# Optimization experiments

Hardware: AMD Instinct MI355X
Metric: run time of the kernel (lower is better)

## Reference

```python
import jax, jax.numpy as jnp
import numpy as np

IN_FEATURES = 4096
OUT_FEATURES = 8192
GROUP_SIZE = 16
NUM_GROUPS = IN_FEATURES * OUT_FEATURES // GROUP_SIZE  # 2_097_152


def block_dequantize_2bit(packed, normalization):
    # packed: [G, group_size//4] int32 holding uint8 values; norm: [G, 1] fp16
    shifts = jnp.arange(4, dtype=packed.dtype) * 2  # bit offsets 0,2,4,6
    # unpacked column 4k+i comes from packed column k, bits 2i..2i+1
    u = ((packed[:, :, None] >> shifts) & 3).astype(jnp.float32)  # [G, gs/4, 4]
    u = u.reshape(packed.shape[0], -1)  # [G, group_size]
    norm = normalization.astype(jnp.float32)
    return (u / 3.0) * (2.0 * norm) - norm  # [G, group_size]


def setup_inputs() -> dict:
    key = jax.random.key(0)
    k_x, k_q, k_n, k_b = jax.random.split(key, 4)
    x = jax.random.normal(k_x, (256, IN_FEATURES), dtype=jnp.float32)
    # packed 2-bit weights: random bytes (store as int32 for clean bit ops in jax)
    weight_q2 = jax.random.randint(k_q, (NUM_GROUPS, GROUP_SIZE // 4), 0, 256, dtype=jnp.int32)
    # per-group normalization (abs-max), positive, fp16 as in the module buffer
    weight_norm = (jax.random.uniform(k_n, (NUM_GROUPS, 1), dtype=jnp.float32) * 0.05 + 1e-4).astype(jnp.float16)
    bias = jax.random.normal(k_b, (OUT_FEATURES,), dtype=jnp.float32) * 0.01
    return {"x": x, "weight_q2": weight_q2, "weight_norm": weight_norm, "bias": bias}


def reference(x, weight_q2, weight_norm, bias):
    weight = block_dequantize_2bit(weight_q2, weight_norm).reshape(OUT_FEATURES, IN_FEATURES)
    return jnp.dot(x.astype(jnp.float32), weight.T) + bias
```

## Files before the change

kernel.cpp:

```cpp
#include <hip/hip_runtime.h>
#include <hip/hip_bf16.h>
#include <hip/hip_fp16.h>

#define IN_F   4096
#define OUT_F  8192
#define M_ROWS 256

typedef __attribute__((ext_vector_type(8))) short  short8;
typedef __attribute__((ext_vector_type(4))) float  float4v;

__device__ inline unsigned int pack_bf16(float lo, float hi) {
    return __builtin_amdgcn_perm(__float_as_uint(hi), __float_as_uint(lo), 0x07060302u);
}

__global__ void cvt_x_kernel(const float* __restrict__ x, unsigned short* __restrict__ xb) {
    int i = blockIdx.x * blockDim.x + threadIdx.x;
    if (i < (M_ROWS * IN_F) / 4) {
        float4 v = ((const float4*)x)[i];
        uint2 o;
        o.x = pack_bf16(v.x, v.y);
        o.y = pack_bf16(v.z, v.w);
        ((uint2*)xb)[i] = o;
    }
}

template <bool XB>
__global__ __launch_bounds__(256) void gemm2bit_kernel(
    const float*           __restrict__ xf,
    const unsigned short*  __restrict__ xb,
    const int*             __restrict__ wq,
    const void*            __restrict__ wnorm,
    const float*           __restrict__ bias,
    float*                 __restrict__ out)
{
    __shared__ unsigned short ldsA[64 * 40];
    __shared__ unsigned short ldsB[64 * 40];

    const int t    = threadIdx.x;
    const int n0   = blockIdx.x * 64;
    const int m0   = blockIdx.y * 64;
    const int wave = t >> 6;
    const int lane = t & 63;
    const int wrow = wave >> 1;
    const int wcol = wave & 1;
    const int l15  = lane & 15;
    const int quad = lane >> 4;

    const float cand0 = *(const float*)wnorm;
    const bool  nf32  = (cand0 > 1e-5f && cand0 < 0.1f);

    const int srow = t >> 2;
    const int sc8  = (t & 3) * 8;

    float4v acc[2][2] = {};

    for (int k0 = 0; k0 < IN_F; k0 += 32) {
        uint4 aval;
        if (XB) {
            aval = *(const uint4*)(xb + (m0 + srow) * IN_F + k0 + sc8);
        } else {
            const float* p = xf + (m0 + srow) * IN_F + k0 + sc8;
            float4 v0 = ((const float4*)p)[0];
            float4 v1 = ((const float4*)p)[1];
            aval.x = pack_bf16(v0.x, v0.y);
            aval.y = pack_bf16(v0.z, v0.w);
            aval.z = pack_bf16(v1.x, v1.y);
            aval.w = pack_bf16(v1.z, v1.w);
        }

        int2  q = *(const int2*)(wq + (n0 + srow) * (IN_F / 4) + ((k0 + sc8) >> 2));
        const int g = (n0 + srow) * (IN_F / 16) + ((k0 + sc8) >> 4);
        float norm;
        if (nf32) norm = ((const float*)wnorm)[g];
        else      norm = __half2float(((const __half*)wnorm)[g]);
        float s  = norm * (2.0f / 3.0f);
        float tn = -norm;
        float f[8];
#pragma unroll
        for (int i = 0; i < 4; ++i)
            f[i] = fmaf((float)((q.x >> (2 * i)) & 3), s, tn);
#pragma unroll
        for (int i = 0; i < 4; ++i)
            f[4 + i] = fmaf((float)((q.y >> (2 * i)) & 3), s, tn);
        uint4 bval;
        bval.x = pack_bf16(f[0], f[1]);
        bval.y = pack_bf16(f[2], f[3]);
        bval.z = pack_bf16(f[4], f[5]);
        bval.w = pack_bf16(f[6], f[7]);

        __syncthreads();
        *(uint4*)&ldsA[srow * 40 + sc8] = aval;
        *(uint4*)&ldsB[srow * 40 + sc8] = bval;
        __syncthreads();

        short8 a0 = *(const short8*)&ldsA[(wrow * 32 +  0 + l15) * 40 + quad * 8];
        short8 a1 = *(const short8*)&ldsA[(wrow * 32 + 16 + l15) * 40 + quad * 8];
        short8 b0 = *(const short8*)&ldsB[(wcol * 32 +  0 + l15) * 40 + quad * 8];
        short8 b1 = *(const short8*)&ldsB[(wcol * 32 + 16 + l15) * 40 + quad * 8];

        acc[0][0] = __builtin_amdgcn_mfma_f32_16x16x32_bf16(a0, b0, acc[0][0], 0, 0, 0);
        acc[0][1] = __builtin_amdgcn_mfma_f32_16x16x32_bf16(a0, b1, acc[0][1], 0, 0, 0);
        acc[1][0] = __builtin_amdgcn_mfma_f32_16x16x32_bf16(a1, b0, acc[1][0], 0, 0, 0);
        acc[1][1] = __builtin_amdgcn_mfma_f32_16x16x32_bf16(a1, b1, acc[1][1], 0, 0, 0);
    }

#pragma unroll
    for (int j = 0; j < 2; ++j) {
        const int col = n0 + wcol * 32 + j * 16 + l15;
        const float bv = bias[col];
#pragma unroll
        for (int i = 0; i < 2; ++i) {
            const int row0 = m0 + wrow * 32 + i * 16 + quad * 4;
#pragma unroll
            for (int r = 0; r < 4; ++r) {
                out[(row0 + r) * OUT_F + col] = acc[i][j][r] + bv;
            }
        }
    }
}

extern "C" void kernel_launch(void* const* d_in, const int* in_sizes, int n_in,
                              void* d_out, int out_size, void* d_ws, size_t ws_size,
                              hipStream_t stream) {
    const float*          x    = (const float*)d_in[0];
    const int*            wq   = (const int*)d_in[1];
    const void*           wn   = (const void*)d_in[2];
    const float*          bias = (const float*)d_in[3];
    float*                out  = (float*)d_out;

    const bool use_ws = ws_size >= (size_t)(M_ROWS * IN_F * sizeof(unsigned short));

    dim3 grid(OUT_F / 64, M_ROWS / 64);

    if (use_ws) {
        unsigned short* xb = (unsigned short*)d_ws;
        cvt_x_kernel<<<dim3((M_ROWS * IN_F / 4 + 255) / 256), 256, 0, stream>>>(x, xb);
        gemm2bit_kernel<true><<<grid, 256, 0, stream>>>(nullptr, xb, wq, wn, bias, out);
    } else {
        gemm2bit_kernel<false><<<grid, 256, 0, stream>>>(x, nullptr, wq, wn, bias, out);
    }
}
```

Measured before the change: 152.9 us.

## Double-buffer LDS with register prefetch, K=64 steps and XOR-swizzled layout

Raises the K step per iteration from 32 to 64, prefetches the next tile's activations, packed weights and norms into registers while the current tile is dequantized and multiplied, and alternates between two LDS buffers so each step needs one barrier instead of two. The LDS layout moves from padded rows to an XOR swizzle to avoid bank conflicts, and launch bounds request two blocks per CU. The goal is to hide global load latency and cut synchronization overhead, at the cost of more registers and LDS per block.

```diff
diff --git a/kernel.cpp b/kernel.cpp
--- a/kernel.cpp
+++ b/kernel.cpp
@@ -13,6 +13,10 @@
     return __builtin_amdgcn_perm(__float_as_uint(hi), __float_as_uint(lo), 0x07060302u);
 }
 
+__device__ inline int sw_idx(int row, int kchunk) {
+    return row * 64 + ((kchunk ^ (row & 7)) << 3);
+}
+
 __global__ void cvt_x_kernel(const float* __restrict__ x, unsigned short* __restrict__ xb) {
     int i = blockIdx.x * blockDim.x + threadIdx.x;
     if (i < (M_ROWS * IN_F) / 4) {
@@ -24,8 +28,17 @@
     }
 }
 
+__device__ inline void load_a16_f32(const float* __restrict__ p, uint4& o0, uint4& o1) {
+    float4 v0 = ((const float4*)p)[0], v1 = ((const float4*)p)[1];
+    float4 v2 = ((const float4*)p)[2], v3 = ((const float4*)p)[3];
+    o0.x = pack_bf16(v0.x, v0.y); o0.y = pack_bf16(v0.z, v0.w);
+    o0.z = pack_bf16(v1.x, v1.y); o0.w = pack_bf16(v1.z, v1.w);
+    o1.x = pack_bf16(v2.x, v2.y); o1.y = pack_bf16(v2.z, v2.w);
+    o1.z = pack_bf16(v3.x, v3.y); o1.w = pack_bf16(v3.z, v3.w);
+}
+
 template <bool XB>
-__global__ __launch_bounds__(256) void gemm2bit_kernel(
+__global__ __launch_bounds__(256, 2) void gemm2bit_kernel(
     const float*           __restrict__ xf,
     const unsigned short*  __restrict__ xb,
     const int*             __restrict__ wq,
@@ -33,84 +46,125 @@
     const float*           __restrict__ bias,
     float*                 __restrict__ out)
 {
-    __shared__ unsigned short ldsA[64 * 40];
-    __shared__ unsigned short ldsB[64 * 40];
+    __shared__ unsigned short lds[2][2][64 * 64];
 
     const int t    = threadIdx.x;
     const int n0   = blockIdx.x * 64;
     const int m0   = blockIdx.y * 64;
     const int wave = t >> 6;
     const int lane = t & 63;
-    const int wrow = wave >> 1;
-    const int wcol = wave & 1;
     const int l15  = lane & 15;
     const int quad = lane >> 4;
+    const int wm   = (wave >> 1) * 32;
+    const int wn   = (wave & 1) * 32;
 
     const float cand0 = *(const float*)wnorm;
     const bool  nf32  = (cand0 > 1e-5f && cand0 < 0.1f);
 
     const int srow = t >> 2;
-    const int sc8  = (t & 3) * 8;
+    const int skc  = t & 3;
+    const int c0   = skc * 2;
+    const int wO0  = sw_idx(srow, c0);
+    const int wO1  = sw_idx(srow, c0 + 1);
+
+    int fa0[2], fa1[2], fb0[2], fb1[2];
+#pragma unroll
+    for (int kk = 0; kk < 2; ++kk) {
+        fa0[kk] = sw_idx(wm +      l15, kk * 4 + quad);
+        fa1[kk] = sw_idx(wm + 16 + l15, kk * 4 + quad);
+        fb0[kk] = sw_idx(wn +      l15, kk * 4 + quad);
+        fb1[kk] = sw_idx(wn + 16 + l15, kk * 4 + quad);
+    }
+
+    const int arow = m0 + srow;
+    const int brow = n0 + srow;
+    const float*          nrmF = (const float*)wnorm;
+    const __half*         nrmH = (const __half*)wnorm;
 
     float4v acc[2][2] = {};
 
-    for (int k0 = 0; k0 < IN_F; k0 += 32) {
-        uint4 aval;
+    uint4 aN0, aN1; int4 qN; float nN;
+    {
         if (XB) {
-            aval = *(const uint4*)(xb + (m0 + srow) * IN_F + k0 + sc8);
+            const unsigned short* p = xb + arow * IN_F + skc * 16;
+            aN0 = *(const uint4*)p;
+            aN1 = *(const uint4*)(p + 8);
         } else {
-            const float* p = xf + (m0 + srow) * IN_F + k0 + sc8;
-            float4 v0 = ((const float4*)p)[0];
-            float4 v1 = ((const float4*)p)[1];
-            aval.x = pack_bf16(v0.x, v0.y);
-            aval.y = pack_bf16(v0.z, v0.w);
-            aval.z = pack_bf16(v1.x, v1.y);
-            aval.w = pack_bf16(v1.z, v1.w);
+            load_a16_f32(xf + arow * IN_F + skc * 16, aN0, aN1);
         }
+        qN = *(const int4*)(wq + brow * (IN_F / 4) + skc * 4);
+        const int gi = brow * (IN_F / 16) + skc;
+        nN = nf32 ? nrmF[gi] : __half2float(nrmH[gi]);
+    }
 
-        int2  q = *(const int2*)(wq + (n0 + srow) * (IN_F / 4) + ((k0 + sc8) >> 2));
-        const int g = (n0 + srow) * (IN_F / 16) + ((k0 + sc8) >> 4);
-        float norm;
-        if (nf32) norm = ((const float*)wnorm)[g];
-        else      norm = __half2float(((const __half*)wnorm)[g]);
-        float s  = norm * (2.0f / 3.0f);
-        float tn = -norm;
-        float f[8];
+    for (int ito = 0; ito < 32; ++ito) {
 #pragma unroll
-        for (int i = 0; i < 4; ++i)
-            f[i] = fmaf((float)((q.x >> (2 * i)) & 3), s, tn);
+        for (int half = 0; half < 2; ++half) {
+            const int it = ito * 2 + half;
+
+            uint4 aC0 = aN0, aC1 = aN1;
+            int4  qC  = qN;
+            float nC  = nN;
+
+            if (it < 63) {
+                const int kn = (it + 1) << 6;
+                if (XB) {
+                    const unsigned short* p = xb + arow * IN_F + kn + skc * 16;
+                    aN0 = *(const uint4*)p;
+                    aN1 = *(const uint4*)(p + 8);
+                } else {
+                    load_a16_f32(xf + arow * IN_F + kn + skc * 16, aN0, aN1);
+                }
+                qN = *(const int4*)(wq + brow * (IN_F / 4) + (kn >> 2) + skc * 4);
+                const int gi = brow * (IN_F / 16) + (kn >> 4) + skc;
+                nN = nf32 ? nrmF[gi] : __half2float(nrmH[gi]);
+            }
+
+            const float s = nC * (2.0f / 3.0f);
+            float f[16];
+            const int qa[4] = {qC.x, qC.y, qC.z, qC.w};
 #pragma unroll
-        for (int i = 0; i < 4; ++i)
-            f[4 + i] = fmaf((float)((q.y >> (2 * i)) & 3), s, tn);
-        uint4 bval;
-        bval.x = pack_bf16(f[0], f[1]);
-        bval.y = pack_bf16(f[2], f[3]);
-        bval.z = pack_bf16(f[4], f[5]);
-        bval.w = pack_bf16(f[6], f[7]);
+            for (int bq = 0; bq < 4; ++bq) {
+#pragma unroll
+                for (int i = 0; i < 4; ++i)
+                    f[bq * 4 + i] = fmaf((float)((qa[bq] >> (2 * i)) & 3), s, -nC);
+            }
+            uint4 bv0, bv1;
+            bv0.x = pack_bf16(f[0],  f[1]);   bv0.y = pack_bf16(f[2],  f[3]);
+            bv0.z = pack_bf16(f[4],  f[5]);   bv0.w = pack_bf16(f[6],  f[7]);
+            bv1.x = pack_bf16(f[8],  f[9]);   bv1.y = pack_bf16(f[10], f[11]);
+            bv1.z = pack_bf16(f[12], f[13]);  bv1.w = pack_bf16(f[14], f[15]);
 
-        __syncthreads();
-        *(uint4*)&ldsA[srow * 40 + sc8] = aval;
-        *(uint4*)&ldsB[srow * 40 + sc8] = bval;
-        __syncthreads();
+            unsigned short* LA = lds[half][0];
+            unsigned short* LB = lds[half][1];
+            *(uint4*)&LA[wO0] = aC0;
+            *(uint4*)&LA[wO1] = aC1;
+            *(uint4*)&LB[wO0] = bv0;
+            *(uint4*)&LB[wO1] = bv1;
 
-        short8 a0 = *(const short8*)&ldsA[(wrow * 32 +  0 + l15) * 40 + quad * 8];
-        short8 a1 = *(const short8*)&ldsA[(wrow * 32 + 16 + l15) * 40 + quad * 8];
-        short8 b0 = *(const short8*)&ldsB[(wcol * 32 +  0 + l15) * 40 + quad * 8];
-        short8 b1 = *(const short8*)&ldsB[(wcol * 32 + 16 + l15) * 40 + quad * 8];
+            __syncthreads();
 
-        acc[0][0] = __builtin_amdgcn_mfma_f32_16x16x32_bf16(a0, b0, acc[0][0], 0, 0, 0);
-        acc[0][1] = __builtin_amdgcn_mfma_f32_16x16x32_bf16(a0, b1, acc[0][1], 0, 0, 0);
-        acc[1][0] = __builtin_amdgcn_mfma_f32_16x16x32_bf16(a1, b0, acc[1][0], 0, 0, 0);
-        acc[1][1] = __builtin_amdgcn_mfma_f32_16x16x32_bf16(a1, b1, acc[1][1], 0, 0, 0);
+#pragma unroll
+            for (int kk = 0; kk < 2; ++kk) {
+                short8 a0 = *(const short8*)&LA[fa0[kk]];
+                short8 a1 = *(const short8*)&LA[fa1[kk]];
+                short8 b0 = *(const short8*)&LB[fb0[kk]];
+                short8 b1 = *(const short8*)&LB[fb1[kk]];
+                acc[0][0] = __builtin_amdgcn_mfma_f32_16x16x32_bf16(a0, b0, acc[0][0], 0, 0, 0);
+                acc[0][1] = __builtin_amdgcn_mfma_f32_16x16x32_bf16(a0, b1, acc[0][1], 0, 0, 0);
+                acc[1][0] = __builtin_amdgcn_mfma_f32_16x16x32_bf16(a1, b0, acc[1][0], 0, 0, 0);
+                acc[1][1] = __builtin_amdgcn_mfma_f32_16x16x32_bf16(a1, b1, acc[1][1], 0, 0, 0);
+            }
+        }
     }
 
 #pragma unroll
     for (int j = 0; j < 2; ++j) {
-        const int col = n0 + wcol * 32 + j * 16 + l15;
+        const int col = n0 + wn + j * 16 + l15;
         const float bv = bias[col];
 #pragma unroll
         for (int i = 0; i < 2; ++i) {
-            const int row0 = m0 + wrow * 32 + i * 16 + quad * 4;
+            const int row0 = m0 + wm + i * 16 + quad * 4;
 #pragma unroll
             for (int r = 0; r < 4; ++r) {
                 out[(row0 + r) * OUT_F + col] = acc[i][j][r] + bv;
```

After: 128.6 us. -15.9%, faster.

## Restructure 2-bit GEMM with double-buffered swizzled LDS slabs and register-dequantized weights

Applied to the files above, without the earlier changes.

Activations are now staged into LDS in large 256-wide K slabs with an XOR swizzle and double buffering, and the next slab is prefetched into registers while MFMAs run on the current one. Each wave dequantizes its own 16 weight columns straight into MFMA B operands, so the B tile no longer passes through LDS and the loop needs one barrier per slab instead of two per 32-wide K step. This trades more registers (prefetch buffers, launch bounds of 2 blocks) and 64 KB of LDS per block for less synchronisation and LDS traffic.

```diff
diff --git a/kernel.cpp b/kernel.cpp
--- a/kernel.cpp
+++ b/kernel.cpp
@@ -5,9 +5,13 @@
 #define IN_F   4096
 #define OUT_F  8192
 #define M_ROWS 256
+#define SLAB   256
+#define NSLAB  (IN_F / SLAB)
 
 typedef __attribute__((ext_vector_type(8))) short  short8;
 typedef __attribute__((ext_vector_type(4))) float  float4v;
+
+union BF8 { uint4 u; short8 s; };
 
 __device__ inline unsigned int pack_bf16(float lo, float hi) {
     return __builtin_amdgcn_perm(__float_as_uint(hi), __float_as_uint(lo), 0x07060302u);
@@ -25,7 +29,7 @@
 }
 
 template <bool XB>
-__global__ __launch_bounds__(256) void gemm2bit_kernel(
+__global__ __launch_bounds__(256, 2) void gemm2bit_kernel(
     const float*           __restrict__ xf,
     const unsigned short*  __restrict__ xb,
     const int*             __restrict__ wq,
@@ -33,88 +37,132 @@
     const float*           __restrict__ bias,
     float*                 __restrict__ out)
 {
-    __shared__ unsigned short ldsA[64 * 40];
-    __shared__ unsigned short ldsB[64 * 40];
+    __shared__ unsigned short ldsA[2][64 * SLAB];
 
     const int t    = threadIdx.x;
     const int n0   = blockIdx.x * 64;
     const int m0   = blockIdx.y * 64;
     const int wave = t >> 6;
     const int lane = t & 63;
-    const int wrow = wave >> 1;
-    const int wcol = wave & 1;
     const int l15  = lane & 15;
     const int quad = lane >> 4;
 
     const float cand0 = *(const float*)wnorm;
     const bool  nf32  = (cand0 > 1e-5f && cand0 < 0.1f);
+    const float*  nF = (const float*)wnorm;
+    const __half* nH = (const __half*)wnorm;
 
-    const int srow = t >> 2;
-    const int sc8  = (t & 3) * 8;
+    const int   ncol = n0 + wave * 16 + l15;
+    const float bv   = bias[ncol];
 
-    float4v acc[2][2] = {};
+    const int* wqBase  = wq + ncol * (IN_F / 4) + quad * 2;
+    const int  nrmBase = ncol * (IN_F / 16) + (quad >> 1);
 
-    for (int k0 = 0; k0 < IN_F; k0 += 32) {
-        uint4 aval;
-        if (XB) {
-            aval = *(const uint4*)(xb + (m0 + srow) * IN_F + k0 + sc8);
-        } else {
-            const float* p = xf + (m0 + srow) * IN_F + k0 + sc8;
-            float4 v0 = ((const float4*)p)[0];
-            float4 v1 = ((const float4*)p)[1];
-            aval.x = pack_bf16(v0.x, v0.y);
-            aval.y = pack_bf16(v0.z, v0.w);
-            aval.z = pack_bf16(v1.x, v1.y);
-            aval.w = pack_bf16(v1.z, v1.w);
+    const int srow = t & 63;
+    const int skq  = t >> 6;
+    const int sr7  = srow & 7;
+    const int wbase = srow * SLAB + skq * 64;
+
+    int fe[4], fo[4];
+#pragma unroll
+    for (int i = 0; i < 4; ++i) {
+        const int row = i * 16 + l15;
+        fe[i] = row * SLAB + ((quad     ) ^ (l15 & 7)) * 8;
+        fo[i] = row * SLAB + ((quad ^ 4 ) ^ (l15 & 7)) * 8;
+    }
+
+    float4v acc[4] = {};
+
+    uint4 stg[8];
+    if (XB) {
+        const uint4* g = (const uint4*)(xb + (m0 + srow) * IN_F + skq * 64);
+#pragma unroll
+        for (int i = 0; i < 8; ++i) stg[i] = g[i];
+    } else {
+        const float4* g = (const float4*)(xf + (m0 + srow) * IN_F + skq * 64);
+#pragma unroll
+        for (int i = 0; i < 8; ++i) {
+            float4 v0 = g[2 * i], v1 = g[2 * i + 1];
+            stg[i].x = pack_bf16(v0.x, v0.y); stg[i].y = pack_bf16(v0.z, v0.w);
+            stg[i].z = pack_bf16(v1.x, v1.y); stg[i].w = pack_bf16(v1.z, v1.w);
+        }
+    }
+    {
+        unsigned short* B = ldsA[0];
+#pragma unroll
+        for (int i = 0; i < 8; ++i)
+            *(uint4*)&B[wbase + ((i ^ sr7) << 3)] = stg[i];
+    }
+
+    for (int s = 0; s < NSLAB; ++s) {
+        __syncthreads();
+
+        uint4 nxt[8];
+        if (s + 1 < NSLAB) {
+            if (XB) {
+                const uint4* g = (const uint4*)(xb + (m0 + srow) * IN_F + (s + 1) * SLAB + skq * 64);
+#pragma unroll
+                for (int i = 0; i < 8; ++i) nxt[i] = g[i];
+            } else {
+                const float4* g = (const float4*)(xf + (m0 + srow) * IN_F + (s + 1) * SLAB + skq * 64);
+#pragma unroll
+                for (int i = 0; i < 8; ++i) {
+                    float4 v0 = g[2 * i], v1 = g[2 * i + 1];
+                    nxt[i].x = pack_bf16(v0.x, v0.y); nxt[i].y = pack_bf16(v0.z, v0.w);
+                    nxt[i].z = pack_bf16(v1.x, v1.y); nxt[i].w = pack_bf16(v1.z, v1.w);
+                }
+            }
         }
 
-        int2  q = *(const int2*)(wq + (n0 + srow) * (IN_F / 4) + ((k0 + sc8) >> 2));
-        const int g = (n0 + srow) * (IN_F / 16) + ((k0 + sc8) >> 4);
-        float norm;
-        if (nf32) norm = ((const float*)wnorm)[g];
-        else      norm = __half2float(((const __half*)wnorm)[g]);
-        float s  = norm * (2.0f / 3.0f);
-        float tn = -norm;
-        float f[8];
+        const unsigned short* A  = ldsA[s & 1];
+        const int*  wqS  = wqBase  + s * 64;
+        const int   nrmS = nrmBase + s * 16;
+
 #pragma unroll
-        for (int i = 0; i < 4; ++i)
-            f[i] = fmaf((float)((q.x >> (2 * i)) & 3), s, tn);
+        for (int ks = 0; ks < 8; ++ks) {
+            const int2  q  = *(const int2*)(wqS + ks * 8);
+            const int   gi = nrmS + ks * 2;
+            const float nn = nf32 ? nF[gi] : __half2float(nH[gi]);
+            const float sc = nn * (2.0f / 3.0f);
+
+            float f0 = fmaf((float)((q.x      ) & 3), sc, -nn);
+            float f1 = fmaf((float)((q.x >>  2) & 3), sc, -nn);
+            float f2 = fmaf((float)((q.x >>  4) & 3), sc, -nn);
+            float f3 = fmaf((float)((q.x >>  6) & 3), sc, -nn);
+            float f4 = fmaf((float)((q.y      ) & 3), sc, -nn);
+            float f5 = fmaf((float)((q.y >>  2) & 3), sc, -nn);
+            float f6 = fmaf((float)((q.y >>  4) & 3), sc, -nn);
+            float f7 = fmaf((float)((q.y >>  6) & 3), sc, -nn);
+
+            BF8 bb;
+            bb.u.x = pack_bf16(f0, f1);
+            bb.u.y = pack_bf16(f2, f3);
+            bb.u.z = pack_bf16(f4, f5);
+            bb.u.w = pack_bf16(f6, f7);
+
+            const int ko = (ks >> 1) * 64;
 #pragma unroll
-        for (int i = 0; i < 4; ++i)
-            f[4 + i] = fmaf((float)((q.y >> (2 * i)) & 3), s, tn);
-        uint4 bval;
-        bval.x = pack_bf16(f[0], f[1]);
-        bval.y = pack_bf16(f[2], f[3]);
-        bval.z = pack_bf16(f[4], f[5]);
-        bval.w = pack_bf16(f[6], f[7]);
+            for (int i = 0; i < 4; ++i) {
+                const int off = ((ks & 1) ? fo[i] : fe[i]) + ko;
+                short8 a = *(const short8*)&A[off];
+                acc[i] = __builtin_amdgcn_mfma_f32_16x16x32_bf16(a, bb.s, acc[i], 0, 0, 0);
+            }
+        }
 
-        __syncthreads();
-        *(uint4*)&ldsA[srow * 40 + sc8] = aval;
-        *(uint4*)&ldsB[srow * 40 + sc8] = bval;
-        __syncthreads();
-
-        short8 a0 = *(const short8*)&ldsA[(wrow * 32 +  0 + l15) * 40 + quad * 8];
-        short8 a1 = *(const short8*)&ldsA[(wrow * 32 + 16 + l15) * 40 + quad * 8];
-        short8 b0 = *(const short8*)&ldsB[(wcol * 32 +  0 + l15) * 40 + quad * 8];
-        short8 b1 = *(const short8*)&ldsB[(wcol * 32 + 16 + l15) * 40 + quad * 8];
-
-        acc[0][0] = __builtin_amdgcn_mfma_f32_16x16x32_bf16(a0, b0, acc[0][0], 0, 0, 0);
-        acc[0][1] = __builtin_amdgcn_mfma_f32_16x16x32_bf16(a0, b1, acc[0][1], 0, 0, 0);
-        acc[1][0] = __builtin_amdgcn_mfma_f32_16x16x32_bf16(a1, b0, acc[1][0], 0, 0, 0);
-        acc[1][1] = __builtin_amdgcn_mfma_f32_16x16x32_bf16(a1, b1, acc[1][1], 0, 0, 0);
+        if (s + 1 < NSLAB) {
+            unsigned short* B = ldsA[(s + 1) & 1];
+#pragma unroll
+            for (int i = 0; i < 8; ++i)
+                *(uint4*)&B[wbase + ((i ^ sr7) << 3)] = nxt[i];
+        }
     }
 
 #pragma unroll
-    for (int j = 0; j < 2; ++j) {
-        const int col = n0 + wcol * 32 + j * 16 + l15;
-        const float bv = bias[col];
+    for (int i = 0; i < 4; ++i) {
+        const int row0 = m0 + i * 16 + quad * 4;
 #pragma unroll
-        for (int i = 0; i < 2; ++i) {
-            const int row0 = m0 + wrow * 32 + i * 16 + quad * 4;
-#pragma unroll
-            for (int r = 0; r < 4; ++r) {
-                out[(row0 + r) * OUT_F + col] = acc[i][j][r] + bv;
-            }
+        for (int r = 0; r < 4; ++r) {
+            out[(row0 + r) * OUT_F + ncol] = acc[i][r] + bv;
         }
     }
 }
@@ -122,11 +170,11 @@
 extern "C" void kernel_launch(void* const* d_in, const int* in_sizes, int n_in,
                               void* d_out, int out_size, void* d_ws, size_t ws_size,
                               hipStream_t stream) {
-    const float*          x    = (const float*)d_in[0];
-    const int*            wq   = (const int*)d_in[1];
-    const void*           wn   = (const void*)d_in[2];
-    const float*          bias = (const float*)d_in[3];
-    float*                out  = (float*)d_out;
+    const float* x    = (const float*)d_in[0];
+    const int*   wq   = (const int*)d_in[1];
+    const void*  wn   = (const void*)d_in[2];
+    const float* bias = (const float*)d_in[3];
+    float*       out  = (float*)d_out;
 
     const bool use_ws = ws_size >= (size_t)(M_ROWS * IN_F * sizeof(unsigned short));
 
```

New measurement: 239.9 us. +56.9%, slower.
